# Kernel tuning notes

Measured on AMD Instinct MI355X. Metric: run time of the kernel, lower is better.

Reference implementation:

```python
import jax, jax.numpy as jnp
import numpy as np

# alpha clamp limits: balance=False -> [exp(-1/5), exp(-1/25)]
ALPHA_MIN = float(np.exp(-1.0 / 5.0))
ALPHA_MAX = float(np.exp(-1.0 / 25.0))
T_CROP = 100


def setup_inputs() -> dict:
    key = jax.random.key(0)
    k1, k2, k3 = jax.random.split(key, 3)
    B, T, D, H = 128, 1000, 1024, 256
    x = jax.random.normal(k1, (B, T, D), dtype=jnp.float32)
    bound = float(np.sqrt(1.0 / D))
    W = jax.random.uniform(k2, (H, D), minval=-bound, maxval=bound, dtype=jnp.float32)
    alpha = jax.random.uniform(k3, (H,), minval=ALPHA_MIN, maxval=ALPHA_MAX, dtype=jnp.float32)
    return {"x": x, "W": W, "alpha": alpha}


def reference(x, W, alpha):
    # x: [B, T, D], W: [H, D], alpha: [H]
    a = jnp.clip(alpha, ALPHA_MIN, ALPHA_MAX)
    Wx = jnp.einsum('btd,hd->bth', x, W)  # [B, T, H]
    T = Wx.shape[1]
    mask = (jnp.arange(T) >= T_CROP).astype(Wx.dtype)  # [T]
    Wx_t = jnp.moveaxis(Wx, 1, 0)  # [T, B, H]

    def step(carry, inp):
        ut, out = carry
        wx, m = inp
        ut = a * ut + (1.0 - a) * wx
        out = out + m * jax.nn.softmax(ut, axis=-1)
        return (ut, out), None

    B, H = Wx.shape[0], Wx.shape[2]
    init = (jnp.zeros((B, H), Wx.dtype), jnp.zeros((B, H), Wx.dtype))
    (_, out), _ = jax.lax.scan(step, init, (Wx_t, mask))
    return out  # [B, H]
```

## Files before the change

### kernel.cpp

```cpp
#include <hip/hip_runtime.h>
#include <hip/hip_bf16.h>

#define B_    128
#define T_    1000
#define D_    1024
#define H_    256
#define TCROP 100
#define CHUNK 25
#define NCHK  40
#define CSKIP 4
#define NOUTC 36
#define BM    125

typedef __attribute__((ext_vector_type(8))) short bfrag8;
typedef __attribute__((ext_vector_type(4))) float f32x4;
typedef unsigned long long ull;

__device__ __forceinline__ float bf2f(unsigned short u) {
    union { unsigned int u; float f; } v; v.u = ((unsigned int)u) << 16;
    return v.f;
}
__device__ __forceinline__ unsigned short f2bf(float f) {
    union { float f; unsigned int u; } v; v.f = f;
    unsigned int u = v.u;
    u += 0x7FFFu + ((u >> 16) & 1u);
    return (unsigned short)(u >> 16);
}
__device__ __forceinline__ unsigned int pack2(float lo, float hi) {
    union { float f; unsigned int u; } a, b; a.f = lo; b.f = hi;
    return __builtin_amdgcn_perm(b.u + 0x8000u, a.u + 0x8000u, 0x07060302u);
}
__device__ __forceinline__ bfrag8 cvt8(float4 f0, float4 f1) {
    union { bfrag8 v; unsigned int u[4]; } r;
    r.u[0] = pack2(f0.x, f0.y);
    r.u[1] = pack2(f0.z, f0.w);
    r.u[2] = pack2(f1.x, f1.y);
    r.u[3] = pack2(f1.z, f1.w);
    return r.v;
}

__global__ __launch_bounds__(256) void wconv_kernel(
        const float* __restrict__ W, unsigned short* __restrict__ Wbf) {
    const int i = (blockIdx.x * 256 + threadIdx.x) * 8;
    float4 f0 = *(const float4*)(W + i);
    float4 f1 = *(const float4*)(W + i + 4);
    *(bfrag8*)(Wbf + i) = cvt8(f0, f1);
}

__global__ __launch_bounds__(512) void gemm_ema_kernel(
        const float* __restrict__ x, const unsigned short* __restrict__ Wbf,
        const float* __restrict__ alpha,
        unsigned short* __restrict__ Wx, float* __restrict__ F) {
    __shared__ unsigned short smem[32000];
    unsigned short* As = smem;
    unsigned short* Bs = smem + 128 * 64;

    const int tid  = threadIdx.x;
    const int lane = tid & 63;
    const int wave = tid >> 6;
    const int wr   = wave >> 2;
    const int wc   = wave & 3;
    const int c    = blockIdx.x;
    const int b    = blockIdx.y;
    const int m0   = b * T_ + c * BM;

    f32x4 acc[4][4];
#pragma unroll
    for (int m = 0; m < 4; ++m)
#pragma unroll
        for (int n = 0; n < 4; ++n) acc[m][n] = (f32x4){0.f, 0.f, 0.f, 0.f};

    const int rr  = lane & 15;
    const int kh  = lane >> 4;
    const int ra0 = tid >> 3;
    const int ja  = tid & 7;
    const int sa  = (ja ^ (ra0 & 7)) * 8;
    const int r1  = (ra0 + 64 <= BM - 1) ? ra0 + 64 : BM - 1;
    const float* ap0 = x + (size_t)(m0 + ra0) * D_ + ja * 8;
    const float* ap1 = x + (size_t)(m0 + r1) * D_ + ja * 8;

    for (int it = 0; it < 16; ++it) {
        const int kt = it * 64;
        float4 f00 = *(const float4*)(ap0 + kt);
        float4 f01 = *(const float4*)(ap0 + kt + 4);
        float4 f10 = *(const float4*)(ap1 + kt);
        float4 f11 = *(const float4*)(ap1 + kt + 4);
#pragma unroll
        for (int q = 0; q < 4; ++q) {
            const int li = q * 512 + tid;
            const int r = li >> 3, j = li & 7;
            const int jj = j ^ (r & 7);
            __builtin_amdgcn_global_load_lds(
                (const __attribute__((address_space(1))) void*)
                    (Wbf + (size_t)r * D_ + kt + jj * 8),
                (__attribute__((address_space(3))) void*)&Bs[li * 8], 16, 0, 0);
        }
        *(bfrag8*)&As[ra0 * 64 + sa]        = cvt8(f00, f01);
        *(bfrag8*)&As[(ra0 + 64) * 64 + sa] = cvt8(f10, f11);
        __syncthreads();
#pragma unroll
        for (int kk = 0; kk < 2; ++kk) {
            const int c16 = kk * 4 + kh;
            bfrag8 af[4], bfr[4];
#pragma unroll
            for (int m = 0; m < 4; ++m) {
                const int row = wr * 64 + m * 16 + rr;
                af[m] = *(const bfrag8*)&As[row * 64 + ((c16 ^ (row & 7)) * 8)];
            }
#pragma unroll
            for (int n = 0; n < 4; ++n) {
                const int row = wc * 64 + n * 16 + rr;
                bfr[n] = *(const bfrag8*)&Bs[row * 64 + ((c16 ^ (row & 7)) * 8)];
            }
#pragma unroll
            for (int m = 0; m < 4; ++m)
#pragma unroll
                for (int n = 0; n < 4; ++n)
                    acc[m][n] = __builtin_amdgcn_mfma_f32_16x16x32_bf16(
                        af[m], bfr[n], acc[m][n], 0, 0, 0);
        }
        __syncthreads();
    }

    const int cl = lane & 15, rg = lane >> 4;
#pragma unroll
    for (int m = 0; m < 4; ++m)
#pragma unroll
        for (int n = 0; n < 4; ++n)
#pragma unroll
            for (int j = 0; j < 4; ++j) {
                const int row = wr * 64 + m * 16 + rg * 4 + j;
                if (row < BM) {
                    const int col = wc * 64 + n * 16 + cl;
                    smem[row * 256 + (col ^ (((row >> 2) & 3) << 4))] =
                        f2bf(acc[m][n][j]);
                }
            }
    __syncthreads();

    if (tid < 256) {
        const int h = tid;
        const float AMIN = 0.81873075307798182f, AMAX = 0.96078943915232320f;
        const float a  = fminf(fmaxf(alpha[h], AMIN), AMAX);
        const float om = 1.0f - a;
        float ut = 0.f;
        const size_t fbase = ((size_t)b * NCHK + c * 5) * H_ + h;
#pragma unroll 5
        for (int r = 0; r < BM; ++r) {
            ut = a * ut + om * bf2f(smem[r * 256 + (h ^ (((r >> 2) & 3) << 4))]);
            if ((r % 25) == 24) {
                F[fbase + (size_t)(r / 25) * H_] = ut;
                ut = 0.f;
            }
        }
    } else {
        const int nrows = (c == 0) ? (BM - TCROP) : BM;
        const int rbase = (c == 0) ? TCROP : 0;
        const int total = nrows * 32;
        for (int li = tid - 256; li < total; li += 256) {
            const int r  = rbase + (li >> 5);
            const int cg = (li & 31) * 8;
            const int scg = cg ^ (((r >> 2) & 3) << 4);
            bfrag8 v = *(const bfrag8*)&smem[r * 256 + scg];
            const int t = c * BM + r;
            *(bfrag8*)&Wx[((size_t)b * T_ + t) * H_ + cg] = v;
        }
    }
}

__global__ __launch_bounds__(256) void scanC_kernel(
        const unsigned short* __restrict__ Wx, const float* __restrict__ alpha,
        const float* __restrict__ F, float* __restrict__ P) {
    const int wave = threadIdx.x >> 6;
    const int lane = threadIdx.x & 63;
    const int c = CSKIP + blockIdx.x * 4 + wave;
    const int b = blockIdx.y;
    const int h4 = lane * 4;

    const float AMIN = 0.81873075307798182f, AMAX = 0.96078943915232320f;
    float4 al = *(const float4*)(alpha + h4);
    float a[4]  = {fminf(fmaxf(al.x, AMIN), AMAX), fminf(fmaxf(al.y, AMIN), AMAX),
                   fminf(fmaxf(al.z, AMIN), AMAX), fminf(fmaxf(al.w, AMIN), AMAX)};
    float om[4] = {1.f - a[0], 1.f - a[1], 1.f - a[2], 1.f - a[3]};

    float aL[4] = {__powf(a[0], (float)CHUNK), __powf(a[1], (float)CHUNK),
                   __powf(a[2], (float)CHUNK), __powf(a[3], (float)CHUNK)};
    float S[4] = {0.f, 0.f, 0.f, 0.f};
    for (int j = 0; j < c; ++j) {
        float4 f = *(const float4*)(F + ((size_t)b * NCHK + j) * H_ + h4);
        S[0] = aL[0] * S[0] + f.x;
        S[1] = aL[1] * S[1] + f.y;
        S[2] = aL[2] * S[2] + f.z;
        S[3] = aL[3] * S[3] + f.w;
    }

    float ut[4]   = {S[0], S[1], S[2], S[3]};
    float acc4[4] = {0.f, 0.f, 0.f, 0.f};
    const unsigned short* base = Wx + ((size_t)b * T_ + c * CHUNK) * H_ + h4;

#pragma unroll
    for (int bb = 0; bb < CHUNK; bb += 5) {
        float e[5][4], sl[5];
#pragma unroll
        for (int q = 0; q < 5; ++q) {
            ull wv = *(const ull*)(base + (size_t)(bb + q) * H_);
            ut[0] = a[0] * ut[0] + om[0] * bf2f((unsigned short)wv);
            ut[1] = a[1] * ut[1] + om[1] * bf2f((unsigned short)(wv >> 16));
            ut[2] = a[2] * ut[2] + om[2] * bf2f((unsigned short)(wv >> 32));
            ut[3] = a[3] * ut[3] + om[3] * bf2f((unsigned short)(wv >> 48));
            e[q][0] = __expf(ut[0]);
            e[q][1] = __expf(ut[1]);
            e[q][2] = __expf(ut[2]);
            e[q][3] = __expf(ut[3]);
            sl[q] = (e[q][0] + e[q][1]) + (e[q][2] + e[q][3]);
        }
#pragma unroll
        for (int dd = 1; dd < 64; dd <<= 1) {
            sl[0] += __shfl_xor(sl[0], dd);
            sl[1] += __shfl_xor(sl[1], dd);
            sl[2] += __shfl_xor(sl[2], dd);
            sl[3] += __shfl_xor(sl[3], dd);
            sl[4] += __shfl_xor(sl[4], dd);
        }
#pragma unroll
        for (int q = 0; q < 5; ++q) {
            const float rcp = 1.0f / sl[q];
            acc4[0] += e[q][0] * rcp;
            acc4[1] += e[q][1] * rcp;
            acc4[2] += e[q][2] * rcp;
            acc4[3] += e[q][3] * rcp;
        }
    }
    float4 o; o.x = acc4[0]; o.y = acc4[1]; o.z = acc4[2]; o.w = acc4[3];
    *(float4*)(P + ((size_t)b * NOUTC + (c - CSKIP)) * H_ + h4) = o;
}

__global__ __launch_bounds__(256) void scanD_kernel(
        const float* __restrict__ P, float* __restrict__ out) {
    const int b = blockIdx.x, h = threadIdx.x;
    float s = 0.f;
#pragma unroll 4
    for (int k = 0; k < NOUTC; ++k) s += P[((size_t)b * NOUTC + k) * H_ + h];
    out[(size_t)b * H_ + h] = s;
}

extern "C" void kernel_launch(void* const* d_in, const int* in_sizes, int n_in,
                              void* d_out, int out_size, void* d_ws, size_t ws_size,
                              hipStream_t stream) {
    const float* x     = (const float*)d_in[0];
    const float* W     = (const float*)d_in[1];
    const float* alpha = (const float*)d_in[2];
    float* out = (float*)d_out;

    char* ws = (char*)d_ws;
    unsigned short* Wbf = (unsigned short*)ws;
    unsigned short* Wx  = (unsigned short*)(ws + ((size_t)1 << 20));
    float* F = (float*)(ws + ((size_t)70 << 20));
    float* P = (float*)(ws + ((size_t)80 << 20));

    wconv_kernel<<<128, 256, 0, stream>>>(W, Wbf);
    gemm_ema_kernel<<<dim3(T_ / BM, B_), 512, 0, stream>>>(x, Wbf, alpha, Wx, F);
    scanC_kernel<<<dim3(NOUTC / 4, B_), 256, 0, stream>>>(Wx, alpha, F, P);
    scanD_kernel<<<B_, 256, 0, stream>>>(P, out);
}
```

Before: 187.3 us.

## Double-buffer fp32 x tiles via direct-to-LDS loads and pre-swizzle W into MFMA fragments

The GEMM now streams fp32 x tiles straight into LDS with global_load_lds, double-buffered so the next K-tile load overlaps the current MFMAs. The bf16 conversion moves to the moment fragments are read from LDS. W is pre-packed by wconv into MFMA-fragment order, so B fragments are read straight from global/L2 and no longer staged in LDS. This removes the register round-trip and the synchronous wait on x loads, at the cost of a larger fp32 LDS footprint (64KB), which may reduce occupancy, plus repeated conversions and uncached-by-LDS B reads.

```diff
diff --git a/kernel.cpp b/kernel.cpp
--- a/kernel.cpp
+++ b/kernel.cpp
@@ -26,34 +26,38 @@
     u += 0x7FFFu + ((u >> 16) & 1u);
     return (unsigned short)(u >> 16);
 }
-__device__ __forceinline__ unsigned int pack2(float lo, float hi) {
-    union { float f; unsigned int u; } a, b; a.f = lo; b.f = hi;
-    return __builtin_amdgcn_perm(b.u + 0x8000u, a.u + 0x8000u, 0x07060302u);
-}
-__device__ __forceinline__ bfrag8 cvt8(float4 f0, float4 f1) {
+__device__ __forceinline__ unsigned int cvtpk2(float lo, float hi) {
+    union { __hip_bfloat162 h; unsigned int u; } v;
+    v.h = __float22bfloat162_rn(make_float2(lo, hi));
+    return v.u;
+}
+
+__global__ __launch_bounds__(256) void wconv_kernel(
+        const float* __restrict__ W, unsigned short* __restrict__ Bfr) {
+    const int g    = blockIdx.x * 256 + threadIdx.x;
+    const int lane = g & 63;
+    const int grp  = g >> 6;
+    const int c16  = grp >> 4;
+    const int hb   = grp & 15;
+    const int row  = hb * 16 + (lane & 15);
+    const int col  = c16 * 32 + (lane >> 4) * 8;
+    const float* src = W + (size_t)row * D_ + col;
+    float4 f0 = *(const float4*)src;
+    float4 f1 = *(const float4*)(src + 4);
     union { bfrag8 v; unsigned int u[4]; } r;
-    r.u[0] = pack2(f0.x, f0.y);
-    r.u[1] = pack2(f0.z, f0.w);
-    r.u[2] = pack2(f1.x, f1.y);
-    r.u[3] = pack2(f1.z, f1.w);
-    return r.v;
-}
-
-__global__ __launch_bounds__(256) void wconv_kernel(
-        const float* __restrict__ W, unsigned short* __restrict__ Wbf) {
-    const int i = (blockIdx.x * 256 + threadIdx.x) * 8;
-    float4 f0 = *(const float4*)(W + i);
-    float4 f1 = *(const float4*)(W + i + 4);
-    *(bfrag8*)(Wbf + i) = cvt8(f0, f1);
+    r.u[0] = cvtpk2(f0.x, f0.y);
+    r.u[1] = cvtpk2(f0.z, f0.w);
+    r.u[2] = cvtpk2(f1.x, f1.y);
+    r.u[3] = cvtpk2(f1.z, f1.w);
+    *(bfrag8*)(Bfr + (size_t)g * 8) = r.v;
 }
 
 __global__ __launch_bounds__(512) void gemm_ema_kernel(
-        const float* __restrict__ x, const unsigned short* __restrict__ Wbf,
+        const float* __restrict__ x, const unsigned short* __restrict__ Bfr,
         const float* __restrict__ alpha,
         unsigned short* __restrict__ Wx, float* __restrict__ F) {
-    __shared__ unsigned short smem[32000];
-    unsigned short* As = smem;
-    unsigned short* Bs = smem + 128 * 64;
+    __shared__ unsigned int smem4[16384];
+    float* As = (float*)smem4;
 
     const int tid  = threadIdx.x;
     const int lane = tid & 63;
@@ -72,45 +76,64 @@
 
     const int rr  = lane & 15;
     const int kh  = lane >> 4;
-    const int ra0 = tid >> 3;
-    const int ja  = tid & 7;
-    const int sa  = (ja ^ (ra0 & 7)) * 8;
-    const int r1  = (ra0 + 64 <= BM - 1) ? ra0 + 64 : BM - 1;
-    const float* ap0 = x + (size_t)(m0 + ra0) * D_ + ja * 8;
-    const float* ap1 = x + (size_t)(m0 + r1) * D_ + ja * 8;
+    const int swz = ((rr & 7) << 1) | (rr >> 3);
+
+    const float* asrc[4];
+    int sdst[4];
+#pragma unroll
+    for (int q = 0; q < 4; ++q) {
+        const int li = q * 512 + tid;
+        const int r  = li >> 4;
+        const int j  = li & 15;
+        const int rs = (r < BM) ? r : (BM - 1);
+        const int js = j ^ (((r & 7) << 1) | ((r >> 3) & 1));
+        asrc[q] = x + (size_t)(m0 + rs) * D_ + js * 4;
+        sdst[q] = li * 4;
+    }
+    int rowoff[4];
+#pragma unroll
+    for (int m = 0; m < 4; ++m) rowoff[m] = (wr * 64 + m * 16 + rr) * 64;
+
+    const unsigned short* bbase = Bfr + ((size_t)(wc * 4) << 9) + lane * 8;
+
+#pragma unroll
+    for (int q = 0; q < 4; ++q)
+        __builtin_amdgcn_global_load_lds(
+            (const __attribute__((address_space(1))) void*)asrc[q],
+            (__attribute__((address_space(3))) void*)&As[sdst[q]], 16, 0, 0);
+    __syncthreads();
 
     for (int it = 0; it < 16; ++it) {
-        const int kt = it * 64;
-        float4 f00 = *(const float4*)(ap0 + kt);
-        float4 f01 = *(const float4*)(ap0 + kt + 4);
-        float4 f10 = *(const float4*)(ap1 + kt);
-        float4 f11 = *(const float4*)(ap1 + kt + 4);
-#pragma unroll
-        for (int q = 0; q < 4; ++q) {
-            const int li = q * 512 + tid;
-            const int r = li >> 3, j = li & 7;
-            const int jj = j ^ (r & 7);
-            __builtin_amdgcn_global_load_lds(
-                (const __attribute__((address_space(1))) void*)
-                    (Wbf + (size_t)r * D_ + kt + jj * 8),
-                (__attribute__((address_space(3))) void*)&Bs[li * 8], 16, 0, 0);
-        }
-        *(bfrag8*)&As[ra0 * 64 + sa]        = cvt8(f00, f01);
-        *(bfrag8*)&As[(ra0 + 64) * 64 + sa] = cvt8(f10, f11);
-        __syncthreads();
+        const int cur = it & 1, nxt = cur ^ 1;
+        if (it < 15) {
+            const int ktn = (it + 1) * 64;
+#pragma unroll
+            for (int q = 0; q < 4; ++q)
+                __builtin_amdgcn_global_load_lds(
+                    (const __attribute__((address_space(1))) void*)(asrc[q] + ktn),
+                    (__attribute__((address_space(3))) void*)
+                        &As[nxt * 8192 + sdst[q]], 16, 0, 0);
+        }
 #pragma unroll
         for (int kk = 0; kk < 2; ++kk) {
-            const int c16 = kk * 4 + kh;
-            bfrag8 af[4], bfr[4];
+            bfrag8 bfr[4];
+            const size_t boff = (size_t)(it * 2 + kk) * 8192;
+#pragma unroll
+            for (int n = 0; n < 4; ++n)
+                bfr[n] = *(const bfrag8*)(bbase + boff + (size_t)n * 512);
+            const int gl = (2 * (kk * 4 + kh)) ^ swz;
+            bfrag8 af[4];
 #pragma unroll
             for (int m = 0; m < 4; ++m) {
-                const int row = wr * 64 + m * 16 + rr;
-                af[m] = *(const bfrag8*)&As[row * 64 + ((c16 ^ (row & 7)) * 8)];
-            }
-#pragma unroll
-            for (int n = 0; n < 4; ++n) {
-                const int row = wc * 64 + n * 16 + rr;
-                bfr[n] = *(const bfrag8*)&Bs[row * 64 + ((c16 ^ (row & 7)) * 8)];
+                const float* pa = As + cur * 8192 + rowoff[m];
+                float4 lo = *(const float4*)(pa + gl * 4);
+                float4 hi = *(const float4*)(pa + (gl ^ 1) * 4);
+                union { bfrag8 v; unsigned int u[4]; } t;
+                t.u[0] = cvtpk2(lo.x, lo.y);
+                t.u[1] = cvtpk2(lo.z, lo.w);
+                t.u[2] = cvtpk2(hi.x, hi.y);
+                t.u[3] = cvtpk2(hi.z, hi.w);
+                af[m] = t.v;
             }
 #pragma unroll
             for (int m = 0; m < 4; ++m)
@@ -122,6 +145,7 @@
         __syncthreads();
     }
 
+    unsigned short* ct = (unsigned short*)smem4;
     const int cl = lane & 15, rg = lane >> 4;
 #pragma unroll
     for (int m = 0; m < 4; ++m)
@@ -132,7 +156,7 @@
                 const int row = wr * 64 + m * 16 + rg * 4 + j;
                 if (row < BM) {
                     const int col = wc * 64 + n * 16 + cl;
-                    smem[row * 256 + (col ^ (((row >> 2) & 3) << 4))] =
+                    ct[row * 256 + (col ^ (((row >> 2) & 3) << 4))] =
                         f2bf(acc[m][n][j]);
                 }
             }
@@ -147,7 +171,7 @@
         const size_t fbase = ((size_t)b * NCHK + c * 5) * H_ + h;
 #pragma unroll 5
         for (int r = 0; r < BM; ++r) {
-            ut = a * ut + om * bf2f(smem[r * 256 + (h ^ (((r >> 2) & 3) << 4))]);
+            ut = a * ut + om * bf2f(ct[r * 256 + (h ^ (((r >> 2) & 3) << 4))]);
             if ((r % 25) == 24) {
                 F[fbase + (size_t)(r / 25) * H_] = ut;
                 ut = 0.f;
@@ -161,7 +185,7 @@
             const int r  = rbase + (li >> 5);
             const int cg = (li & 31) * 8;
             const int scg = cg ^ (((r >> 2) & 3) << 4);
-            bfrag8 v = *(const bfrag8*)&smem[r * 256 + scg];
+            bfrag8 v = *(const bfrag8*)&ct[r * 256 + scg];
             const int t = c * BM + r;
             *(bfrag8*)&Wx[((size_t)b * T_ + t) * H_ + cg] = v;
         }
@@ -253,13 +277,13 @@
     float* out = (float*)d_out;
 
     char* ws = (char*)d_ws;
-    unsigned short* Wbf = (unsigned short*)ws;
+    unsigned short* Bfr = (unsigned short*)ws;
     unsigned short* Wx  = (unsigned short*)(ws + ((size_t)1 << 20));
     float* F = (float*)(ws + ((size_t)70 << 20));
     float* P = (float*)(ws + ((size_t)80 << 20));
 
-    wconv_kernel<<<128, 256, 0, stream>>>(W, Wbf);
-    gemm_ema_kernel<<<dim3(T_ / BM, B_), 512, 0, stream>>>(x, Wbf, alpha, Wx, F);
+    wconv_kernel<<<128, 256, 0, stream>>>(W, Bfr);
+    gemm_ema_kernel<<<dim3(T_ / BM, B_), 512, 0, stream>>>(x, Bfr, alpha, Wx, F);
     scanC_kernel<<<dim3(NOUTC / 4, B_), 256, 0, stream>>>(Wx, alpha, F, P);
     scanD_kernel<<<B_, 256, 0, stream>>>(P, out);
 }
```

Result: slower. 205.6 us (+9.8%).
